# Performance work log

Measured on AMD Instinct MI355X. Metric: run time of the kernel, lower is better.

## Reference

```python
import jax, jax.numpy as jnp
import numpy as np

EPS = 1e-12
B, CNT = 4096, 2048

def setup_inputs() -> dict:
    key = jax.random.key(0)
    k1, k2, k3 = jax.random.split(key, 3)
    timestampns_set = jax.random.uniform(k1, (B, CNT), dtype=jnp.float32)
    gyro_set = jax.random.normal(k2, (B, CNT, 3), dtype=jnp.float32)
    start_quat = jax.random.normal(k3, (B, 4), dtype=jnp.float32)
    # conv1/conv2 reduce to 3x3 linear maps on the xyz axis; initialized to identity, bias 0
    W1 = jnp.eye(3, dtype=jnp.float32)
    b1 = jnp.zeros((3,), dtype=jnp.float32)
    a1 = jnp.float32(0.25)  # PReLU default, single shared parameter
    W2 = jnp.eye(3, dtype=jnp.float32)
    b2 = jnp.zeros((3,), dtype=jnp.float32)
    a2 = jnp.float32(0.25)
    return {"timestampns_set": timestampns_set, "gyro_set": gyro_set,
            "start_quat": start_quat, "W1": W1, "b1": b1, "a1": a1,
            "W2": W2, "b2": b2, "a2": a2}

def _prelu(x, a):
    return jnp.where(x >= 0, x, a * x)

def _qmul(a, b):
    aw, ax, ay, az = a[:, 0], a[:, 1], a[:, 2], a[:, 3]
    bw, bx, by, bz = b[:, 0], b[:, 1], b[:, 2], b[:, 3]
    ow = aw * bw - ax * bx - ay * by - az * bz
    ox = aw * bx + ax * bw + ay * bz - az * by
    oy = aw * by - ax * bz + ay * bw + az * bx
    oz = aw * bz + ax * by - ay * bx + az * bw
    return jnp.stack((ow, ox, oy, oz), axis=-1)

def reference(timestampns_set, gyro_set, start_quat, W1, b1, a1, W2, b2, a2):
    # calibrate_gyro: two identity-init 3x3 'convs' + PReLU, residual add
    h = _prelu(jnp.einsum('btc,oc->bto', gyro_set, W1) + b1, a1)
    g = _prelu(jnp.einsum('btc,oc->bto', h, W2) + b2, a2) + gyro_set  # [B,CNT,3]
    dt = timestampns_set[:, 1:] - timestampns_set[:, :-1]             # [B,CNT-1]
    gm = 0.5 * (g[:, :-1, :] + g[:, 1:, :])                            # midpoint gyro
    dtheta_half = gm * dt[:, :, None] * 0.5                           # [B,CNT-1,3]

    def step(q, d):
        dq = jnp.concatenate([jnp.ones((d.shape[0], 1), d.dtype), d], axis=1)
        q = _qmul(q, dq)
        n = jnp.sqrt(jnp.sum(q * q, axis=1, keepdims=True))
        q = q / jnp.maximum(n, EPS)  # F.normalize semantics
        return q, None

    q, _ = jax.lax.scan(step, start_quat, jnp.swapaxes(dtheta_half, 0, 1))
    return q
```

## Files before the change

kernel.cpp:

```cpp
#include <hip/hip_runtime.h>

#define CNT   2048
#define TPB   256
#define RPB   4
#define NMAC  4
#define MAC   8

struct Q { float w, x, y, z; };

__device__ __forceinline__ Q qmul(const Q a, const Q b) {
    Q o;
    o.w = fmaf(a.w, b.w, fmaf(-a.x, b.x, fmaf(-a.y, b.y, -a.z * b.z)));
    o.x = fmaf(a.w, b.x, fmaf( a.x, b.w, fmaf( a.y, b.z, -a.z * b.y)));
    o.y = fmaf(a.w, b.y, fmaf(-a.x, b.z, fmaf( a.y, b.w,  a.z * b.x)));
    o.z = fmaf(a.w, b.z, fmaf( a.x, b.y, fmaf(-a.y, b.x,  a.z * b.w)));
    return o;
}

__device__ __forceinline__ Q qmul1(const Q a, const float bx, const float by, const float bz) {
    Q o;
    o.w = fmaf(-a.x, bx, fmaf(-a.y, by, fmaf(-a.z, bz, a.w)));
    o.x = fmaf( a.w, bx, fmaf( a.y, bz, fmaf(-a.z, by, a.x)));
    o.y = fmaf( a.w, by, fmaf(-a.x, bz, fmaf( a.z, bx, a.y)));
    o.z = fmaf( a.w, bz, fmaf( a.x, by, fmaf(-a.y, bx, a.z)));
    return o;
}

__device__ __forceinline__ float prelu(const float x, const float a, const float one_m_a) {
    return fmaf(one_m_a, fmaxf(x, 0.0f), a * x);
}

__global__ __launch_bounds__(TPB) void quat_scan_kernel(
    const float* __restrict__ ts,
    const float* __restrict__ gyro,
    const float* __restrict__ sq,
    const float* __restrict__ W1, const float* __restrict__ b1, const float* __restrict__ a1p,
    const float* __restrict__ W2, const float* __restrict__ b2, const float* __restrict__ a2p,
    float* __restrict__ out,
    const int B)
{
    const int lane = threadIdx.x & 63;
    const int wid  = threadIdx.x >> 6;
    const int row  = blockIdx.x * RPB + wid;
    if (row >= B) return;

    float w1[9], w2[9], bb1[3], bb2[3];
    #pragma unroll
    for (int i = 0; i < 9; ++i) { w1[i] = W1[i]; w2[i] = W2[i]; }
    #pragma unroll
    for (int i = 0; i < 3; ++i) { bb1[i] = b1[i]; bb2[i] = b2[i]; }
    const float a1 = a1p[0], a2 = a2p[0];
    const float oma1 = 1.0f - a1, oma2 = 1.0f - a2;

    auto gfv = [&](const float vx, const float vy, const float vz,
                   float& gx, float& gy, float& gz) {
        float h0 = fmaf(w1[0], vx, fmaf(w1[1], vy, fmaf(w1[2], vz, bb1[0])));
        float h1 = fmaf(w1[3], vx, fmaf(w1[4], vy, fmaf(w1[5], vz, bb1[1])));
        float h2 = fmaf(w1[6], vx, fmaf(w1[7], vy, fmaf(w1[8], vz, bb1[2])));
        h0 = prelu(h0, a1, oma1);
        h1 = prelu(h1, a1, oma1);
        h2 = prelu(h2, a1, oma1);
        float u0 = fmaf(w2[0], h0, fmaf(w2[1], h1, fmaf(w2[2], h2, bb2[0])));
        float u1 = fmaf(w2[3], h0, fmaf(w2[4], h1, fmaf(w2[5], h2, bb2[1])));
        float u2 = fmaf(w2[6], h0, fmaf(w2[7], h1, fmaf(w2[8], h2, bb2[2])));
        gx = prelu(u0, a2, oma2) + vx;
        gy = prelu(u1, a2, oma2) + vy;
        gz = prelu(u2, a2, oma2) + vz;
    };

    const float4* gp = (const float4*)(gyro + (size_t)row * (CNT * 3));
    const float4* tp = (const float4*)(ts   + (size_t)row * CNT);
    const int gbase = 24 * lane;
    const int tbase = 8  * lane;

    Q q = {1.0f, 0.0f, 0.0f, 0.0f};
    float g0x, g0y, g0z;

    #pragma unroll
    for (int m = 0; m < NMAC; ++m) {
        float4 Gv[7];
        #pragma unroll
        for (int k = 0; k < 7; ++k) {
            int gi = gbase + 6 * m + k;
            gi = gi > (CNT * 3 / 4 - 1) ? (CNT * 3 / 4 - 1) : gi;
            Gv[k] = gp[gi];
        }
        float4 Tv[3];
        #pragma unroll
        for (int k = 0; k < 3; ++k) {
            int ti = tbase + 2 * m + k;
            ti = ti > (CNT / 4 - 1) ? (CNT / 4 - 1) : ti;
            Tv[k] = tp[ti];
        }

        float gg[28];
        #pragma unroll
        for (int k = 0; k < 7; ++k) {
            gg[4*k+0] = Gv[k].x; gg[4*k+1] = Gv[k].y;
            gg[4*k+2] = Gv[k].z; gg[4*k+3] = Gv[k].w;
        }
        float rtw[12];
        #pragma unroll
        for (int k = 0; k < 3; ++k) {
            rtw[4*k+0] = Tv[k].x; rtw[4*k+1] = Tv[k].y;
            rtw[4*k+2] = Tv[k].z; rtw[4*k+3] = Tv[k].w;
        }
        if (m == NMAC - 1) rtw[8] = (lane == 63) ? rtw[7] : rtw[8];

        if (m == 0) gfv(gg[0], gg[1], gg[2], g0x, g0y, g0z);

        #pragma unroll
        for (int u = 0; u < MAC; ++u) {
            float g1x, g1y, g1z;
            gfv(gg[3*u+3], gg[3*u+4], gg[3*u+5], g1x, g1y, g1z);
            const float s = 0.25f * (rtw[u + 1] - rtw[u]);
            q = qmul1(q, (g0x + g1x) * s, (g0y + g1y) * s, (g0z + g1z) * s);
            g0x = g1x; g0y = g1y; g0z = g1z;
        }
    }

    {
        const float n2  = fmaf(q.w, q.w, fmaf(q.x, q.x, fmaf(q.y, q.y, q.z * q.z)));
        const float inv = 1.0f / sqrtf(n2);
        q.w *= inv; q.x *= inv; q.y *= inv; q.z *= inv;
    }

    #pragma unroll
    for (int sft = 1; sft < 64; sft <<= 1) {
        Q o;
        o.w = __shfl_down(q.w, sft);
        o.x = __shfl_down(q.x, sft);
        o.y = __shfl_down(q.y, sft);
        o.z = __shfl_down(q.z, sft);
        q = qmul(q, o);
    }

    if (lane == 0) {
        const float4 s0 = ((const float4*)(sq + (size_t)row * 4))[0];
        const Q q0 = {s0.x, s0.y, s0.z, s0.w};
        Q qf = qmul(q0, q);
        const float n   = sqrtf(fmaf(qf.w, qf.w, fmaf(qf.x, qf.x, fmaf(qf.y, qf.y, qf.z * qf.z))));
        const float inv = 1.0f / fmaxf(n, 1e-12f);
        float4 o;
        o.x = qf.w * inv; o.y = qf.x * inv; o.z = qf.y * inv; o.w = qf.z * inv;
        ((float4*)(out + (size_t)row * 4))[0] = o;
    }
}

extern "C" void kernel_launch(void* const* d_in, const int* in_sizes, int n_in,
                              void* d_out, int out_size, void* d_ws, size_t ws_size,
                              hipStream_t stream) {
    const float* ts   = (const float*)d_in[0];
    const float* gyro = (const float*)d_in[1];
    const float* sq   = (const float*)d_in[2];
    const float* W1   = (const float*)d_in[3];
    const float* b1   = (const float*)d_in[4];
    const float* a1   = (const float*)d_in[5];
    const float* W2   = (const float*)d_in[6];
    const float* b2   = (const float*)d_in[7];
    const float* a2   = (const float*)d_in[8];
    float* out = (float*)d_out;

    const int B = in_sizes[0] / CNT;
    const int grid = (B + RPB - 1) / RPB;

    quat_scan_kernel<<<grid, TPB, 0, stream>>>(ts, gyro, sq, W1, b1, a1, W2, b2, a2, out, B);
}
```

Measured before the change: 202.5 us.

## Stream row data through double-buffered LDS via async global-to-LDS loads

The kernel now splits each row into 8 chunks of 256 steps. Each chunk's gyro and timestamp data is prefetched two chunks ahead with global_load_lds into a per-wave double buffer in shared memory. Each lane integrates 4 steps per chunk, and the chunk quaternions are combined with a shuffle tree and accumulated across chunks. The aim is to overlap memory latency with compute instead of issuing all register loads up front. In exchange it adds eight shuffle reductions per row, uses 32 KB of LDS per block, and relies on manual vmcnt waits.

```diff
diff --git a/kernel.cpp b/kernel.cpp
--- a/kernel.cpp
+++ b/kernel.cpp
@@ -1,10 +1,12 @@
 #include <hip/hip_runtime.h>
 
-#define CNT   2048
-#define TPB   256
-#define RPB   4
-#define NMAC  4
-#define MAC   8
+#define CNT    2048
+#define TPB    256
+#define RPB    4
+#define NCHUNK 8
+#define CSTEP  256
+#define GFL    768
+#define BUFF   1028
 
 struct Q { float w, x, y, z; };
 
@@ -30,6 +32,16 @@
     return fmaf(one_m_a, fmaxf(x, 0.0f), a * x);
 }
 
+__device__ __forceinline__ void dma16(const float* g, float* l) {
+    __builtin_amdgcn_global_load_lds(
+        (const __attribute__((address_space(1))) void*)g,
+        (__attribute__((address_space(3))) void*)l,
+        16, 0, 0);
+}
+
+#define WAITV(n) do { asm volatile("s_waitcnt vmcnt(" #n ")" ::: "memory"); \
+                      __builtin_amdgcn_sched_barrier(0); } while (0)
+
 __global__ __launch_bounds__(TPB) void quat_scan_kernel(
     const float* __restrict__ ts,
     const float* __restrict__ gyro,
@@ -39,6 +51,8 @@
     float* __restrict__ out,
     const int B)
 {
+    __shared__ float lds[RPB][2][BUFF];
+
     const int lane = threadIdx.x & 63;
     const int wid  = threadIdx.x >> 6;
     const int row  = blockIdx.x * RPB + wid;
@@ -68,77 +82,92 @@
         gz = prelu(u2, a2, oma2) + vz;
     };
 
-    const float4* gp = (const float4*)(gyro + (size_t)row * (CNT * 3));
-    const float4* tp = (const float4*)(ts   + (size_t)row * CNT);
-    const int gbase = 24 * lane;
-    const int tbase = 8  * lane;
+    const float* grow = gyro + (size_t)row * (CNT * 3);
+    const float* trow = ts   + (size_t)row * CNT;
+    float* buf0 = &lds[wid][0][0];
+    float* buf1 = &lds[wid][1][0];
 
-    Q q = {1.0f, 0.0f, 0.0f, 0.0f};
-    float g0x, g0y, g0z;
+    auto issue = [&](const int c, float* bp) {
+        const float* gs = grow + c * GFL + lane * 4;
+        dma16(gs +   0, bp +   0);
+        dma16(gs + 256, bp + 256);
+        dma16(gs + 512, bp + 512);
+        dma16(trow + c * CSTEP + lane * 4, bp + GFL);
+    };
 
-    #pragma unroll
-    for (int m = 0; m < NMAC; ++m) {
-        float4 Gv[7];
-        #pragma unroll
-        for (int k = 0; k < 7; ++k) {
-            int gi = gbase + 6 * m + k;
-            gi = gi > (CNT * 3 / 4 - 1) ? (CNT * 3 / 4 - 1) : gi;
-            Gv[k] = gp[gi];
+    issue(0, buf0);
+    issue(1, buf1);
+
+    Q acc = {1.0f, 0.0f, 0.0f, 0.0f};
+
+    WAITV(4);
+
+    for (int c = 0; c < NCHUNK; ++c) {
+        float* cur = (c & 1) ? buf1 : buf0;
+        float* oth = (c & 1) ? buf0 : buf1;
+
+        const float4* gb = (const float4*)cur;
+        const float4* tb = (const float4*)(cur + GFL);
+        const float4 Wa = gb[3 * lane + 0];
+        const float4 Wb = gb[3 * lane + 1];
+        const float4 Wc = gb[3 * lane + 2];
+        const float4 Wd = gb[3 * lane + 3];
+        const float4 Ta = tb[lane];
+        const float4 Tb = tb[lane + 1];
+
+        Q q = {1.0f, 0.0f, 0.0f, 0.0f};
+        float ax, ay, az, bx, by, bz;
+        gfv(Wa.x, Wa.y, Wa.z, ax, ay, az);
+        gfv(Wa.w, Wb.x, Wb.y, bx, by, bz);
+        { const float s = 0.25f * (Ta.y - Ta.x);
+          q = qmul1(q, (ax + bx) * s, (ay + by) * s, (az + bz) * s); }
+        ax = bx; ay = by; az = bz;
+        gfv(Wb.z, Wb.w, Wc.x, bx, by, bz);
+        { const float s = 0.25f * (Ta.z - Ta.y);
+          q = qmul1(q, (ax + bx) * s, (ay + by) * s, (az + bz) * s); }
+        ax = bx; ay = by; az = bz;
+        gfv(Wc.y, Wc.z, Wc.w, bx, by, bz);
+        { const float s = 0.25f * (Ta.w - Ta.z);
+          q = qmul1(q, (ax + bx) * s, (ay + by) * s, (az + bz) * s); }
+        ax = bx; ay = by; az = bz;
+
+        WAITV(0);
+        float rx = Wd.x, ry = Wd.y, rz = Wd.z, t4 = Tb.x;
+        if (c < NCHUNK - 1) {
+            const float4 Xg = ((const float4*)oth)[0];
+            const float  Xt = oth[GFL];
+            if (lane == 63) { rx = Xg.x; ry = Xg.y; rz = Xg.z; t4 = Xt; }
+        } else {
+            if (lane == 63) t4 = Ta.w;
         }
-        float4 Tv[3];
-        #pragma unroll
-        for (int k = 0; k < 3; ++k) {
-            int ti = tbase + 2 * m + k;
-            ti = ti > (CNT / 4 - 1) ? (CNT / 4 - 1) : ti;
-            Tv[k] = tp[ti];
+        gfv(rx, ry, rz, bx, by, bz);
+        { const float s = 0.25f * (t4 - Ta.w);
+          q = qmul1(q, (ax + bx) * s, (ay + by) * s, (az + bz) * s); }
+
+        {
+            const float n2  = fmaf(q.w, q.w, fmaf(q.x, q.x, fmaf(q.y, q.y, q.z * q.z)));
+            const float inv = 1.0f / sqrtf(n2);
+            q.w *= inv; q.x *= inv; q.y *= inv; q.z *= inv;
         }
 
-        float gg[28];
         #pragma unroll
-        for (int k = 0; k < 7; ++k) {
-            gg[4*k+0] = Gv[k].x; gg[4*k+1] = Gv[k].y;
-            gg[4*k+2] = Gv[k].z; gg[4*k+3] = Gv[k].w;
+        for (int sft = 1; sft < 64; sft <<= 1) {
+            Q o;
+            o.w = __shfl_down(q.w, sft);
+            o.x = __shfl_down(q.x, sft);
+            o.y = __shfl_down(q.y, sft);
+            o.z = __shfl_down(q.z, sft);
+            q = qmul(q, o);
         }
-        float rtw[12];
-        #pragma unroll
-        for (int k = 0; k < 3; ++k) {
-            rtw[4*k+0] = Tv[k].x; rtw[4*k+1] = Tv[k].y;
-            rtw[4*k+2] = Tv[k].z; rtw[4*k+3] = Tv[k].w;
-        }
-        if (m == NMAC - 1) rtw[8] = (lane == 63) ? rtw[7] : rtw[8];
+        acc = qmul(acc, q);
 
-        if (m == 0) gfv(gg[0], gg[1], gg[2], g0x, g0y, g0z);
-
-        #pragma unroll
-        for (int u = 0; u < MAC; ++u) {
-            float g1x, g1y, g1z;
-            gfv(gg[3*u+3], gg[3*u+4], gg[3*u+5], g1x, g1y, g1z);
-            const float s = 0.25f * (rtw[u + 1] - rtw[u]);
-            q = qmul1(q, (g0x + g1x) * s, (g0y + g1y) * s, (g0z + g1z) * s);
-            g0x = g1x; g0y = g1y; g0z = g1z;
-        }
-    }
-
-    {
-        const float n2  = fmaf(q.w, q.w, fmaf(q.x, q.x, fmaf(q.y, q.y, q.z * q.z)));
-        const float inv = 1.0f / sqrtf(n2);
-        q.w *= inv; q.x *= inv; q.y *= inv; q.z *= inv;
-    }
-
-    #pragma unroll
-    for (int sft = 1; sft < 64; sft <<= 1) {
-        Q o;
-        o.w = __shfl_down(q.w, sft);
-        o.x = __shfl_down(q.x, sft);
-        o.y = __shfl_down(q.y, sft);
-        o.z = __shfl_down(q.z, sft);
-        q = qmul(q, o);
+        if (c < NCHUNK - 2) issue(c + 2, cur);
     }
 
     if (lane == 0) {
         const float4 s0 = ((const float4*)(sq + (size_t)row * 4))[0];
         const Q q0 = {s0.x, s0.y, s0.z, s0.w};
-        Q qf = qmul(q0, q);
+        Q qf = qmul(q0, acc);
         const float n   = sqrtf(fmaf(qf.w, qf.w, fmaf(qf.x, qf.x, fmaf(qf.y, qf.y, qf.z * qf.z))));
         const float inv = 1.0f / fmaxf(n, 1e-12f);
         float4 o;
```

New measurement: 192.6 us. 1.05x faster.
